# Kernel optimization log

Hardware: AMD Instinct MI355X
Metric: run time of the kernel (lower is better)

The kernel has to match this reference:

```python
import jax, jax.numpy as jnp
import numpy as np

AX = (-2, -1)
LAMBDA = 0.05
ITERS = 6

# torch fft_2d_img  = fftshift(ifft2(ifftshift(x)))  (used in the FORWARD model)
# torch ifft_2d_img = ifftshift(fft2(fftshift(x)))   (used in the ADJOINT model)

def _fwd_xform(x):
    return jnp.fft.fftshift(jnp.fft.ifft2(jnp.fft.ifftshift(x, axes=AX), axes=AX, norm='ortho'), axes=AX)

def _adj_xform(x):
    return jnp.fft.ifftshift(jnp.fft.fft2(jnp.fft.fftshift(x, axes=AX), axes=AX, norm='ortho'), axes=AX)

def _forward_model(img, S, mask):
    # img [b,t,h,w] -> masked multicoil k-space [b,t,c,h,w]
    return mask * _fwd_xform(S * img[:, :, None])

def _adjoint_model(k, S):
    # k [b,t,c,h,w] -> coil-combined image [b,t,h,w]
    return jnp.sum(jnp.conj(S) * _adj_xform(k), axis=2)

def _system_matrix_R(p, S, L, mask):
    # p [b,sv,h,w]; L [b,t,sv]
    expanded = jnp.einsum('bts,bshw->bthw', L, p)
    combined = _adjoint_model(_forward_model(expanded, S, mask), S)
    out = jnp.einsum('bts,bthw->bshw', jnp.conj(L), combined)
    return out + LAMBDA * p

def _cg_solve(b_vec, S, L, mask):
    z0 = jnp.zeros_like(b_vec)
    rs0 = jnp.vdot(b_vec, b_vec)

    def step(carry, _):
        z, r, p, rs_old, done = carry
        Ap = _system_matrix_R(p, S, L, mask)
        alpha = rs_old / (jnp.vdot(p, Ap) + 1e-20)
        z_n = z + alpha * p
        r_n = r - alpha * Ap
        rs_new = jnp.vdot(r_n, r_n)
        p_n = r_n + (rs_new / (rs_old + 1e-20)) * p
        # replicate torch early-break: freeze state once residual is tiny
        z_o = jnp.where(done, z, z_n)
        r_o = jnp.where(done, r, r_n)
        p_o = jnp.where(done, p, p_n)
        rs_o = jnp.where(done, rs_old, rs_new)
        done_n = done | (jnp.abs(rs_o) < 1e-10)
        return (z_o, r_o, p_o, rs_o, done_n), None

    carry0 = (z0, b_vec, b_vec, rs0, jnp.array(False))
    (z, _, _, _, _), _ = jax.lax.scan(step, carry0, None, length=ITERS)
    return z

def setup_inputs() -> dict:
    key = jax.random.key(0)
    ks = jax.random.split(key, 9)
    b, t, c, h, w, sv = 2, 12, 10, 256, 256, 3
    f32 = jnp.float32
    inp = {
        'k_real': jax.random.normal(ks[0], (b, t, c, h, w), f32),
        'k_imag': jax.random.normal(ks[1], (b, t, c, h, w), f32),
        'mo_real': jax.random.normal(ks[2], (b, sv, h, w), f32),
        'mo_imag': jax.random.normal(ks[3], (b, sv, h, w), f32),
        's_real': jax.random.normal(ks[4], (b, 1, c, h, w), f32),
        's_imag': jax.random.normal(ks[5], (b, 1, c, h, w), f32),
        'tb_real': jax.random.normal(ks[6], (b, t, sv), f32),
        'tb_imag': jax.random.normal(ks[7], (b, t, sv), f32),
        'mask': (jax.random.uniform(ks[8], (b, t, 1, h, w)) < 0.35).astype(f32),
    }
    return inp

def reference(k_real, k_imag, mo_real, mo_imag, s_real, s_imag, tb_real, tb_imag, mask):
    Y = k_real + 1j * k_imag          # [b,t,c,h,w]
    MO = mo_real + 1j * mo_imag       # [b,sv,h,w]
    S = s_real + 1j * s_imag          # [b,1,c,h,w]
    L = tb_real + 1j * tb_imag        # [b,t,sv]
    # b = L^H A^H Y + lambda * model_output
    b_vec = jnp.einsum('bts,bthw->bshw', jnp.conj(L), _adjoint_model(Y, S)) + LAMBDA * MO
    z = _cg_solve(b_vec, S, L, mask)  # [b,sv,h,w] complex
    return jnp.stack([z.real, z.imag], axis=-1)  # [b,sv,h,w,2] float32
```

## Files before the change

kernel.cpp:

```cpp
#include <hip/hip_runtime.h>
#include <math.h>

#define HW 65536
#define LAM 0.05f

struct Scal {
  double pap_re, pap_im, rs_acc, rs_old;
  int done, cnt;
};

__device__ __forceinline__ float2 cadd(float2 a, float2 b){ return make_float2(a.x+b.x, a.y+b.y); }
__device__ __forceinline__ float2 csub(float2 a, float2 b){ return make_float2(a.x-b.x, a.y-b.y); }
__device__ __forceinline__ float2 cmul(float2 a, float2 b){
  return make_float2(a.x*b.x - a.y*b.y, a.x*b.y + a.y*b.x);
}
__device__ __forceinline__ float2 cmulj(float2 a, float2 b){
  return make_float2(a.x*b.x + a.y*b.y, a.x*b.y - a.y*b.x);
}
__device__ __forceinline__ int swz(int p){ return p ^ (p>>4); }

__device__ __forceinline__ void wave_lds_sync(){
  __builtin_amdgcn_wave_barrier();
  __asm__ __volatile__("s_waitcnt lgkmcnt(0)" ::: "memory");
  __builtin_amdgcn_wave_barrier();
}

template<int S>
__device__ __forceinline__ void bfly4(float2 x0, float2 x1, float2 x2, float2 x3,
                                      float2& y0, float2& y1, float2& y2, float2& y3){
  float2 a  = cadd(x0,x2), bm = csub(x0,x2);
  float2 c  = cadd(x1,x3), d  = csub(x1,x3);
  float2 jd = make_float2(-(float)S*d.y, (float)S*d.x);
  y0 = cadd(a,c); y2 = csub(a,c); y1 = cadd(bm,jd); y3 = csub(bm,jd);
}

template<int S>
__device__ __forceinline__ void dft16(float2* a){
  const float s_ = (float)S;
  const float2 W1 = make_float2( 0.92387953251f,  s_*0.38268343236f);
  const float2 W2 = make_float2( 0.70710678119f,  s_*0.70710678119f);
  const float2 W3 = make_float2( 0.38268343236f,  s_*0.92387953251f);
  const float2 W4_ = make_float2(0.f,              s_*1.f);
  const float2 W6 = make_float2(-0.70710678119f,  s_*0.70710678119f);
  const float2 W9 = make_float2(-0.92387953251f, -s_*0.38268343236f);
  float2 t[16];
#pragma unroll
  for (int n0=0;n0<4;n0++){
    float2 y0,y1,y2,y3;
    bfly4<S>(a[n0], a[n0+4], a[n0+8], a[n0+12], y0,y1,y2,y3);
    if (n0==1){ y1=cmul(y1,W1); y2=cmul(y2,W2); y3=cmul(y3,W3); }
    if (n0==2){ y1=cmul(y1,W2); y2=cmul(y2,W4_); y3=cmul(y3,W6); }
    if (n0==3){ y1=cmul(y1,W3); y2=cmul(y2,W6); y3=cmul(y3,W9); }
    t[n0*4+0]=y0; t[n0*4+1]=y1; t[n0*4+2]=y2; t[n0*4+3]=y3;
  }
#pragma unroll
  for (int k1=0;k1<4;k1++){
    float2 y0,y1,y2,y3;
    bfly4<S>(t[0*4+k1], t[1*4+k1], t[2*4+k1], t[3*4+k1], y0,y1,y2,y3);
    a[k1+0]=y0; a[k1+4]=y1; a[k1+8]=y2; a[k1+12]=y3;
  }
}

template<int S>
__device__ void fft256_r16(float2* buf, int l){
  float2 a[16];
#pragma unroll
  for (int j=0;j<16;j++) a[j] = buf[swz(l + 16*j)];
  dft16<S>(a);
  float ang = (float)S * 6.2831853071795865f * (float)l * (1.f/256.f);
  float sn, cs; __sincosf(ang, &sn, &cs);
  float2 wstep = make_float2(cs, sn);
  float2 w = wstep;
#pragma unroll
  for (int k=1;k<16;k++){ a[k] = cmul(a[k], w); w = cmul(w, wstep); }
#pragma unroll
  for (int k=0;k<16;k++) buf[swz(16*k + l)] = a[k];
  wave_lds_sync();
#pragma unroll
  for (int j=0;j<16;j++) a[j] = buf[swz(16*l + j)];
  dft16<S>(a);
  wave_lds_sync();
#pragma unroll
  for (int k=0;k<16;k++) buf[swz(l + 16*k)] = a[k];
  wave_lds_sync();
}

__global__ __launch_bounds__(256) void k_w(const float* __restrict__ mask,
                                           const float* __restrict__ tbr,
                                           const float* __restrict__ tbi,
                                           float2* __restrict__ Wb,
                                           Scal* sc){
  if (blockIdx.x==0 && blockIdx.y==0 && threadIdx.x==0){
    sc->pap_re=0.0; sc->pap_im=0.0; sc->rs_acc=0.0; sc->rs_old=0.0;
    sc->done=0; sc->cnt=0;
  }
  __shared__ float2 wt[9][16][17];
  int tid = threadIdx.x;
  int bx = blockIdx.x;
  int b  = blockIdx.y;
  int u0 = (bx>>4)<<4, v0 = (bx&15)<<4;
  int u_l = tid>>4, v_l = tid&15;
  int pix = (u0+u_l)*256 + (v0+v_l);
  float d0=0,d1=0,d2=0, o01r=0,o01i=0, o02r=0,o02i=0, o12r=0,o12i=0;
#pragma unroll
  for (int t=0;t<12;t++){
    float m = mask[(size_t)(b*12+t)*HW + pix];
    int lb = (b*12+t)*3;
    float l0r = tbr[lb+0], l0i = tbi[lb+0];
    float l1r = tbr[lb+1], l1i = tbi[lb+1];
    float l2r = tbr[lb+2], l2i = tbi[lb+2];
    d0 += m*(l0r*l0r + l0i*l0i);
    d1 += m*(l1r*l1r + l1i*l1i);
    d2 += m*(l2r*l2r + l2i*l2i);
    o01r += m*(l0r*l1r + l0i*l1i); o01i += m*(l0r*l1i - l0i*l1r);
    o02r += m*(l0r*l2r + l0i*l2i); o02i += m*(l0r*l2i - l0i*l2r);
    o12r += m*(l1r*l2r + l1i*l2i); o12i += m*(l1r*l2i - l1i*l2r);
  }
  const float s = 1.0f/65536.0f;
  wt[0][u_l][v_l] = make_float2(d0*s, 0.f);
  wt[1][u_l][v_l] = make_float2(o01r*s,  o01i*s);
  wt[2][u_l][v_l] = make_float2(o02r*s,  o02i*s);
  wt[3][u_l][v_l] = make_float2(o01r*s, -o01i*s);
  wt[4][u_l][v_l] = make_float2(d1*s, 0.f);
  wt[5][u_l][v_l] = make_float2(o12r*s,  o12i*s);
  wt[6][u_l][v_l] = make_float2(o02r*s, -o02i*s);
  wt[7][u_l][v_l] = make_float2(o12r*s, -o12i*s);
  wt[8][u_l][v_l] = make_float2(d2*s, 0.f);
  __syncthreads();
  int u_l2 = tid&15, v_l2 = tid>>4;
#pragma unroll
  for (int k=0;k<9;k++){
    Wb[ ((size_t)(b*9+k)*256 + (v0+v_l2))*256 + (u0+u_l2) ] = wt[k][u_l2][v_l2];
  }
}

__global__ __launch_bounds__(512) void k_yrow(const float* __restrict__ kr,
                                              const float* __restrict__ ki,
                                              const float* __restrict__ tbr,
                                              const float* __restrict__ tbi,
                                              float2* __restrict__ bufA){
  __shared__ float2 lb[30*257];
  int tid = threadIdx.x;
  int wv = tid>>6, lane = tid&63, g = lane>>4, l = lane&15;
  int px = tid & 255, half = tid >> 8;
  int r = blockIdx.x, b = blockIdx.y;
  float sg = (((r ^ px) & 1) ? -1.f : 1.f) * (1.f/256.f);
  int sk = swz(px);
#pragma unroll
  for (int cc=0; cc<5; cc++){
    int c = half*5 + cc;
    float a0r=0,a0i=0,a1r=0,a1i=0,a2r=0,a2i=0;
#pragma unroll
    for (int t=0;t<12;t++){
      size_t off = ((size_t)((b*12+t)*10+c))*HW + (size_t)r*256 + px;
      float yr = kr[off], yi = ki[off];
      int lbi = (b*12+t)*3;
      float l0r = tbr[lbi+0], l0i = tbi[lbi+0];
      float l1r = tbr[lbi+1], l1i = tbi[lbi+1];
      float l2r = tbr[lbi+2], l2i = tbi[lbi+2];
      a0r += l0r*yr + l0i*yi;  a0i += l0r*yi - l0i*yr;
      a1r += l1r*yr + l1i*yi;  a1i += l1r*yi - l1i*yr;
      a2r += l2r*yr + l2i*yi;  a2i += l2r*yi - l2i*yr;
    }
    lb[(c*3+0)*257 + sk] = make_float2(a0r*sg, a0i*sg);
    lb[(c*3+1)*257 + sk] = make_float2(a1r*sg, a1i*sg);
    lb[(c*3+2)*257 + sk] = make_float2(a2r*sg, a2i*sg);
  }
  __syncthreads();
  int tau = 4*wv + g;
  if (tau < 30){
    float2* lw = &lb[tau*257];
    fft256_r16<-1>(lw, l);
    float2* dst = bufA + (size_t)(b*30+tau)*HW + (size_t)r*256;
#pragma unroll
    for (int j=0;j<8;j++){
      int e = 2*(16*j + l);
      float2 e0 = lw[swz(e)], e1 = lw[swz(e+1)];
      *(float4*)(dst + e) = make_float4(e0.x,e0.y,e1.x,e1.y);
    }
  }
}

template<int MODE>
__global__ __launch_bounds__(384) void k_colpass(float2* __restrict__ bufA,
                                                 const float2* __restrict__ Wb){
  __shared__ float2 lb[24*257];
  int tid = threadIdx.x;
  int wv = tid>>6, lane = tid&63, g = lane>>4, l = lane&15;
  int j0 = blockIdx.x*8;
  int c = blockIdx.y, b = blockIdx.z;
#pragma unroll
  for (int it=0; it<8; it++){
    int idx = it*384 + tid;
    int s = idx>>10, rem = idx&1023, u = rem>>2, cp = rem&3;
    const float2* src = bufA + (size_t)(b*30 + c*3 + s)*HW;
    float4 v = *(const float4*)(src + u*256 + j0 + 2*cp);
    lb[(s*8+2*cp  )*257 + swz(u)] = make_float2(v.x, v.y);
    lb[(s*8+2*cp+1)*257 + swz(u)] = make_float2(v.z, v.w);
  }
  __syncthreads();
  int tau = 4*wv + g;
  if (MODE==0){
    fft256_r16<-1>(&lb[tau*257], l);
  } else {
    fft256_r16<1>(&lb[tau*257], l);
    __syncthreads();
    const float2* Wp = Wb + (size_t)b*9*HW;
    for (int idx=tid; idx<2048; idx+=384){
      int u = idx&255, col = idx>>8;
      int su = swz(u);
      int v = j0 + col;
      float2 x0 = lb[(0*8+col)*257 + su];
      float2 x1 = lb[(1*8+col)*257 + su];
      float2 x2 = lb[(2*8+col)*257 + su];
      size_t wb = (size_t)v*256 + u;
      float2 y0 = cmul(Wp[(size_t)0*HW + wb], x0);
      y0 = cadd(y0, cmul(Wp[(size_t)1*HW + wb], x1));
      y0 = cadd(y0, cmul(Wp[(size_t)2*HW + wb], x2));
      float2 y1 = cmul(Wp[(size_t)3*HW + wb], x0);
      y1 = cadd(y1, cmul(Wp[(size_t)4*HW + wb], x1));
      y1 = cadd(y1, cmul(Wp[(size_t)5*HW + wb], x2));
      float2 y2 = cmul(Wp[(size_t)6*HW + wb], x0);
      y2 = cadd(y2, cmul(Wp[(size_t)7*HW + wb], x1));
      y2 = cadd(y2, cmul(Wp[(size_t)8*HW + wb], x2));
      lb[(0*8+col)*257 + su] = y0;
      lb[(1*8+col)*257 + su] = y1;
      lb[(2*8+col)*257 + su] = y2;
    }
    __syncthreads();
    fft256_r16<-1>(&lb[tau*257], l);
  }
  __syncthreads();
#pragma unroll
  for (int it=0; it<8; it++){
    int idx = it*384 + tid;
    int s = idx>>10, rem = idx&1023, u = rem>>2, cp = rem&3;
    float2* dst = bufA + (size_t)(b*30 + c*3 + s)*HW;
    float2 e0 = lb[(s*8+2*cp  )*257 + swz(u)];
    float2 e1 = lb[(s*8+2*cp+1)*257 + swz(u)];
    *(float4*)(dst + u*256 + j0 + 2*cp) = make_float4(e0.x, e0.y, e1.x, e1.y);
  }
}

__global__ __launch_bounds__(256) void k_combine(const float2* __restrict__ bufA,
                                                 const float* __restrict__ sr_,
                                                 const float* __restrict__ si_,
                                                 const float* __restrict__ mor,
                                                 const float* __restrict__ moi,
                                                 float2* __restrict__ bvec,
                                                 Scal* sc){
  __shared__ double sd[4];
  int tid = threadIdx.x;
  int i = blockIdx.x*256 + tid;
  int pix = i & (HW-1);
  int bs = i >> 16;
  int b = bs/3, s = bs - 3*b;
  float2 acc = make_float2(0.f, 0.f);
#pragma unroll
  for (int c=0;c<10;c++){
    float2 F  = bufA[(size_t)(b*30 + c*3 + s)*HW + pix];
    size_t so = (size_t)(b*10+c)*HW + pix;
    float2 sv = make_float2(sr_[so], si_[so]);
    acc = cadd(acc, cmulj(sv, F));
  }
  float sgl = (((pix>>8)^pix)&1 ? -1.f : 1.f) * LAM;
  acc.x += sgl*mor[i]; acc.y += sgl*moi[i];
  bvec[i] = acc;
  double dre = (double)acc.x*acc.x + (double)acc.y*acc.y;
  for (int off=32; off>0; off>>=1) dre += __shfl_down(dre, off, 64);
  if ((tid&63)==0) sd[tid>>6] = dre;
  __syncthreads();
  if (tid==0) atomicAdd(&sc->rs_acc, sd[0]+sd[1]+sd[2]+sd[3]);
}

__global__ __launch_bounds__(512) void k_spfft(float2* __restrict__ p,
                                               const float2* __restrict__ rvec,
                                               const float* __restrict__ sr_,
                                               const float* __restrict__ si_,
                                               float2* __restrict__ bufA,
                                               Scal* sc, int first){
  __shared__ float2 lb[30*257];
  int tid = threadIdx.x;
  int wv = tid>>6, lane = tid&63, g = lane>>4, l = lane&15;
  int r = blockIdx.x, b = blockIdx.y;
  if (tid < 256){
    int px = tid, sk = swz(px);
    int done = sc->done;
    float beta = first ? 0.f : (float)(sc->rs_acc / (sc->rs_old + 1e-20));
    float2 pv[3];
#pragma unroll
    for (int s=0;s<3;s++){
      size_t oi = (size_t)(b*3+s)*HW + (size_t)r*256 + px;
      if (!first && !done){
        float2 po = p[oi], rv = rvec[oi];
        float2 pn = make_float2(rv.x + beta*po.x, rv.y + beta*po.y);
        p[oi] = pn; pv[s] = pn;
      } else {
        pv[s] = p[oi];
      }
    }
#pragma unroll
    for (int c=0;c<10;c++){
      size_t so = (size_t)(b*10+c)*HW + (size_t)r*256 + px;
      float2 sv = make_float2(sr_[so], si_[so]);
      lb[(c*3+0)*257 + sk] = cmul(sv, pv[0]);
      lb[(c*3+1)*257 + sk] = cmul(sv, pv[1]);
      lb[(c*3+2)*257 + sk] = cmul(sv, pv[2]);
    }
  }
  __syncthreads();
  int tau = 4*wv + g;
  if (tau < 30){
    float2* lw = &lb[tau*257];
    fft256_r16<1>(lw, l);
    float2* dst = bufA + (size_t)(b*30+tau)*HW + (size_t)r*256;
#pragma unroll
    for (int j=0;j<8;j++){
      int e = 2*(16*j + l);
      float2 e0 = lw[swz(e)], e1 = lw[swz(e+1)];
      *(float4*)(dst + e) = make_float4(e0.x,e0.y,e1.x,e1.y);
    }
  }
  if (tid==0){
    int total = (int)(gridDim.x*gridDim.y);
    int prev = atomicAdd(&sc->cnt, 1);
    if (prev == total-1){
      sc->cnt = 0;
      if (!first && !sc->done){
        sc->rs_old = sc->rs_acc;
        if (fabs(sc->rs_old) < 1e-10) sc->done = 1;
      }
      sc->pap_re = 0.0; sc->pap_im = 0.0; sc->rs_acc = 0.0;
    }
  }
}

__global__ __launch_bounds__(512) void k_rowcomb(const float2* __restrict__ bufA,
                                                 const float* __restrict__ sr_,
                                                 const float* __restrict__ si_,
                                                 const float2* __restrict__ pvec,
                                                 float2* __restrict__ Ap,
                                                 Scal* sc){
  __shared__ float2 lb[30*257];
  __shared__ double sd[8], sd2[8];
  int tid = threadIdx.x;
  int wv = tid>>6, lane = tid&63, g = lane>>4, l = lane&15;
  int r = blockIdx.x, b = blockIdx.y;
  int tau = 4*wv + g;
  if (tau < 30){
    const float2* src = bufA + (size_t)(b*30+tau)*HW + (size_t)r*256;
    float2* lw = &lb[tau*257];
#pragma unroll
    for (int j=0;j<8;j++){
      int e = 2*(16*j + l);
      float4 v = *(const float4*)(src + e);
      lw[swz(e)]   = make_float2(v.x, v.y);
      lw[swz(e+1)] = make_float2(v.z, v.w);
    }
    wave_lds_sync();
    fft256_r16<-1>(lw, l);
  }
  __syncthreads();
  double dre = 0.0, dim = 0.0;
  if (tid < 256){
    int px = tid, sk = swz(px);
    float2 a0={0,0}, a1={0,0}, a2={0,0};
#pragma unroll
    for (int c=0;c<10;c++){
      size_t so = (size_t)(b*10+c)*HW + (size_t)r*256 + px;
      float2 sv = make_float2(sr_[so], si_[so]);
      a0 = cadd(a0, cmulj(sv, lb[(c*3+0)*257 + sk]));
      a1 = cadd(a1, cmulj(sv, lb[(c*3+1)*257 + sk]));
      a2 = cadd(a2, cmulj(sv, lb[(c*3+2)*257 + sk]));
    }
    float2 accs[3] = {a0,a1,a2};
#pragma unroll
    for (int s=0;s<3;s++){
      size_t oi = (size_t)(b*3+s)*HW + (size_t)r*256 + px;
      float2 acc = accs[s];
      float2 av = pvec[oi];
      acc.x += LAM*av.x; acc.y += LAM*av.y;
      Ap[oi] = acc;
      dre += (double)av.x*acc.x + (double)av.y*acc.y;
      dim += (double)av.x*acc.y - (double)av.y*acc.x;
    }
  }
  for (int off=32; off>0; off>>=1){
    dre += __shfl_down(dre, off, 64);
    dim += __shfl_down(dim, off, 64);
  }
  if (lane==0){ sd[wv]=dre; sd2[wv]=dim; }
  __syncthreads();
  if (tid==0){
    double tre=0.0, tim=0.0;
#pragma unroll
    for (int q=0;q<8;q++){ tre+=sd[q]; tim+=sd2[q]; }
    atomicAdd(&sc->pap_re, tre);
    atomicAdd(&sc->pap_im, tim);
  }
}

__global__ __launch_bounds__(256) void k_cginit(const float2* __restrict__ bvec,
                                                float2* __restrict__ z,
                                                float2* __restrict__ r,
                                                float2* __restrict__ p,
                                                Scal* sc){
  int i = blockIdx.x*256 + threadIdx.x;
  float2 bv = bvec[i];
  z[i] = make_float2(0.f,0.f);
  r[i] = bv; p[i] = bv;
  if (i==0){ sc->rs_old = sc->rs_acc; sc->pap_re=0.0; sc->pap_im=0.0; }
}

__global__ __launch_bounds__(256) void k_upzr(float2* __restrict__ z,
                                              float2* __restrict__ r,
                                              const float2* __restrict__ p,
                                              const float2* __restrict__ Ap,
                                              Scal* sc){
  __shared__ double sd[4];
  int tid = threadIdx.x;
  int i = blockIdx.x*256 + tid;
  int done = sc->done;
  double local = 0.0;
  if (!done){
    double dre = sc->pap_re + 1e-20, dim = sc->pap_im;
    double den = dre*dre + dim*dim;
    double rs = sc->rs_old;
    float2 alpha = make_float2((float)( rs*dre/den), (float)(-rs*dim/den));
    float2 pv = p[i], apv = Ap[i];
    float2 zv = cadd(z[i], cmul(alpha, pv));
    float2 rv = csub(r[i], cmul(alpha, apv));
    z[i] = zv; r[i] = rv;
    local = (double)rv.x*rv.x + (double)rv.y*rv.y;
  }
  for (int off=32; off>0; off>>=1) local += __shfl_down(local, off, 64);
  if ((tid&63)==0) sd[tid>>6] = local;
  __syncthreads();
  if (tid==0 && !done){
    atomicAdd(&sc->rs_acc, sd[0]+sd[1]+sd[2]+sd[3]);
  }
}

__global__ __launch_bounds__(256) void k_out(const float2* __restrict__ z,
                                             float* __restrict__ out){
  int i = blockIdx.x*256 + threadIdx.x;
  int pix = i & (HW-1);
  float sgn = (((pix>>8)^pix)&1) ? -1.f : 1.f;
  float2 zv = z[i];
  out[2*i]   = sgn*zv.x;
  out[2*i+1] = sgn*zv.y;
}

extern "C" void kernel_launch(void* const* d_in, const int* in_sizes, int n_in,
                              void* d_out, int out_size, void* d_ws, size_t ws_size,
                              hipStream_t stream){
  const float* kr   = (const float*)d_in[0];
  const float* ki   = (const float*)d_in[1];
  const float* mor  = (const float*)d_in[2];
  const float* moi  = (const float*)d_in[3];
  const float* sr   = (const float*)d_in[4];
  const float* si   = (const float*)d_in[5];
  const float* tbr  = (const float*)d_in[6];
  const float* tbi  = (const float*)d_in[7];
  const float* mask = (const float*)d_in[8];
  float* out = (float*)d_out;

  float2* ws   = (float2*)d_ws;
  float2* bufA = ws;
  float2* Wb   = ws + 3932160;
  float2* bvec = ws + 5111808;
  float2* z    = ws + 5505024;
  float2* r    = ws + 5898240;
  float2* p    = ws + 6291456;
  float2* Ap   = ws + 6684672;
  Scal*   sc   = (Scal*)(ws + 7077888);

  k_w<<<dim3(256,2),dim3(256),0,stream>>>(mask, tbr, tbi, Wb, sc);
  k_yrow<<<dim3(256,2),dim3(512),0,stream>>>(kr, ki, tbr, tbi, bufA);
  k_colpass<0><<<dim3(32,10,2),dim3(384),0,stream>>>(bufA, Wb);
  k_combine<<<dim3(1536),dim3(256),0,stream>>>(bufA, sr, si, mor, moi, bvec, sc);
  k_cginit<<<dim3(1536),dim3(256),0,stream>>>(bvec, z, r, p, sc);
  for (int it=0; it<6; ++it){
    k_spfft<<<dim3(256,2),dim3(512),0,stream>>>(p, r, sr, si, bufA, sc, it==0 ? 1 : 0);
    k_colpass<1><<<dim3(32,10,2),dim3(384),0,stream>>>(bufA, Wb);
    k_rowcomb<<<dim3(256,2),dim3(512),0,stream>>>(bufA, sr, si, p, Ap, sc);
    k_upzr<<<dim3(1536),dim3(256),0,stream>>>(z, r, p, Ap, sc);
  }
  k_out<<<dim3(1536),dim3(256),0,stream>>>(z, out);
}
```

Before: 750.3 us.

## Fuse CG vector updates into spfft, compute rs_new algebraically, store Hermitian weights compactly

Removes the separate z/r update kernel and the cginit kernel. The alpha, beta and rs_new scalars are now computed in the last block of k_rowcomb from the extra dot products r·Ap and Ap·Ap, using the expansion |r-αAp|². The z/r/p updates are deferred into the next k_spfft and into k_out. The 3x3 weight matrix is stored as 9 real floats that exploit its Hermitian symmetry, instead of 9 complex values, which halves the weight reads in colpass. The algebraic rs_new can lose precision through cancellation compared with the directly computed norm.

```diff
diff --git a/kernel.cpp b/kernel.cpp
--- a/kernel.cpp
+++ b/kernel.cpp
@@ -5,8 +5,9 @@
 #define LAM 0.05f
 
 struct Scal {
-  double pap_re, pap_im, rs_acc, rs_old;
-  int done, cnt;
+  double pap_re, pap_im, rq_re, rq_im, qq;
+  double rs_old, al_re, al_im, beta;
+  int done, apply, cnt, pad;
 };
 
 __device__ __forceinline__ float2 cadd(float2 a, float2 b){ return make_float2(a.x+b.x, a.y+b.y); }
@@ -88,13 +89,14 @@
 __global__ __launch_bounds__(256) void k_w(const float* __restrict__ mask,
                                            const float* __restrict__ tbr,
                                            const float* __restrict__ tbi,
-                                           float2* __restrict__ Wb,
+                                           float* __restrict__ Wf,
                                            Scal* sc){
   if (blockIdx.x==0 && blockIdx.y==0 && threadIdx.x==0){
-    sc->pap_re=0.0; sc->pap_im=0.0; sc->rs_acc=0.0; sc->rs_old=0.0;
-    sc->done=0; sc->cnt=0;
-  }
-  __shared__ float2 wt[9][16][17];
+    sc->pap_re=0.0; sc->pap_im=0.0; sc->rq_re=0.0; sc->rq_im=0.0; sc->qq=0.0;
+    sc->rs_old=0.0; sc->al_re=0.0; sc->al_im=0.0; sc->beta=0.0;
+    sc->done=0; sc->apply=0; sc->cnt=0;
+  }
+  __shared__ float wtf[9][16][17];
   int tid = threadIdx.x;
   int bx = blockIdx.x;
   int b  = blockIdx.y;
@@ -117,20 +119,15 @@
     o12r += m*(l1r*l2r + l1i*l2i); o12i += m*(l1r*l2i - l1i*l2r);
   }
   const float s = 1.0f/65536.0f;
-  wt[0][u_l][v_l] = make_float2(d0*s, 0.f);
-  wt[1][u_l][v_l] = make_float2(o01r*s,  o01i*s);
-  wt[2][u_l][v_l] = make_float2(o02r*s,  o02i*s);
-  wt[3][u_l][v_l] = make_float2(o01r*s, -o01i*s);
-  wt[4][u_l][v_l] = make_float2(d1*s, 0.f);
-  wt[5][u_l][v_l] = make_float2(o12r*s,  o12i*s);
-  wt[6][u_l][v_l] = make_float2(o02r*s, -o02i*s);
-  wt[7][u_l][v_l] = make_float2(o12r*s, -o12i*s);
-  wt[8][u_l][v_l] = make_float2(d2*s, 0.f);
+  wtf[0][u_l][v_l] = d0*s;   wtf[1][u_l][v_l] = d1*s;   wtf[2][u_l][v_l] = d2*s;
+  wtf[3][u_l][v_l] = o01r*s; wtf[4][u_l][v_l] = o01i*s;
+  wtf[5][u_l][v_l] = o02r*s; wtf[6][u_l][v_l] = o02i*s;
+  wtf[7][u_l][v_l] = o12r*s; wtf[8][u_l][v_l] = o12i*s;
   __syncthreads();
   int u_l2 = tid&15, v_l2 = tid>>4;
 #pragma unroll
-  for (int k=0;k<9;k++){
-    Wb[ ((size_t)(b*9+k)*256 + (v0+v_l2))*256 + (u0+u_l2) ] = wt[k][u_l2][v_l2];
+  for (int f=0;f<9;f++){
+    Wf[ ((size_t)(b*9+f)*256 + (v0+v_l2))*256 + (u0+u_l2) ] = wtf[f][u_l2][v_l2];
   }
 }
 
@@ -183,7 +180,7 @@
 
 template<int MODE>
 __global__ __launch_bounds__(384) void k_colpass(float2* __restrict__ bufA,
-                                                 const float2* __restrict__ Wb){
+                                                 const float* __restrict__ Wf){
   __shared__ float2 lb[24*257];
   int tid = threadIdx.x;
   int wv = tid>>6, lane = tid&63, g = lane>>4, l = lane&15;
@@ -205,7 +202,7 @@
   } else {
     fft256_r16<1>(&lb[tau*257], l);
     __syncthreads();
-    const float2* Wp = Wb + (size_t)b*9*HW;
+    const float* W0 = Wf + (size_t)b*9*HW;
     for (int idx=tid; idx<2048; idx+=384){
       int u = idx&255, col = idx>>8;
       int su = swz(u);
@@ -214,15 +211,19 @@
       float2 x1 = lb[(1*8+col)*257 + su];
       float2 x2 = lb[(2*8+col)*257 + su];
       size_t wb = (size_t)v*256 + u;
-      float2 y0 = cmul(Wp[(size_t)0*HW + wb], x0);
-      y0 = cadd(y0, cmul(Wp[(size_t)1*HW + wb], x1));
-      y0 = cadd(y0, cmul(Wp[(size_t)2*HW + wb], x2));
-      float2 y1 = cmul(Wp[(size_t)3*HW + wb], x0);
-      y1 = cadd(y1, cmul(Wp[(size_t)4*HW + wb], x1));
-      y1 = cadd(y1, cmul(Wp[(size_t)5*HW + wb], x2));
-      float2 y2 = cmul(Wp[(size_t)6*HW + wb], x0);
-      y2 = cadd(y2, cmul(Wp[(size_t)7*HW + wb], x1));
-      y2 = cadd(y2, cmul(Wp[(size_t)8*HW + wb], x2));
+      float d0  = W0[(size_t)0*HW + wb];
+      float d1  = W0[(size_t)1*HW + wb];
+      float d2  = W0[(size_t)2*HW + wb];
+      float o01r= W0[(size_t)3*HW + wb], o01i = W0[(size_t)4*HW + wb];
+      float o02r= W0[(size_t)5*HW + wb], o02i = W0[(size_t)6*HW + wb];
+      float o12r= W0[(size_t)7*HW + wb], o12i = W0[(size_t)8*HW + wb];
+      float2 y0, y1, y2;
+      y0.x = d0*x0.x + o01r*x1.x - o01i*x1.y + o02r*x2.x - o02i*x2.y;
+      y0.y = d0*x0.y + o01r*x1.y + o01i*x1.x + o02r*x2.y + o02i*x2.x;
+      y1.x = o01r*x0.x + o01i*x0.y + d1*x1.x + o12r*x2.x - o12i*x2.y;
+      y1.y = o01r*x0.y - o01i*x0.x + d1*x1.y + o12r*x2.y + o12i*x2.x;
+      y2.x = o02r*x0.x + o02i*x0.y + o12r*x1.x + o12i*x1.y + d2*x2.x;
+      y2.y = o02r*x0.y - o02i*x0.x + o12r*x1.y - o12i*x1.x + d2*x2.y;
       lb[(0*8+col)*257 + su] = y0;
       lb[(1*8+col)*257 + su] = y1;
       lb[(2*8+col)*257 + su] = y2;
@@ -247,7 +248,9 @@
                                                  const float* __restrict__ si_,
                                                  const float* __restrict__ mor,
                                                  const float* __restrict__ moi,
-                                                 float2* __restrict__ bvec,
+                                                 float2* __restrict__ z,
+                                                 float2* __restrict__ r,
+                                                 float2* __restrict__ p,
                                                  Scal* sc){
   __shared__ double sd[4];
   int tid = threadIdx.x;
@@ -265,39 +268,46 @@
   }
   float sgl = (((pix>>8)^pix)&1 ? -1.f : 1.f) * LAM;
   acc.x += sgl*mor[i]; acc.y += sgl*moi[i];
-  bvec[i] = acc;
+  z[i] = make_float2(0.f,0.f);
+  r[i] = acc; p[i] = acc;
   double dre = (double)acc.x*acc.x + (double)acc.y*acc.y;
   for (int off=32; off>0; off>>=1) dre += __shfl_down(dre, off, 64);
   if ((tid&63)==0) sd[tid>>6] = dre;
   __syncthreads();
-  if (tid==0) atomicAdd(&sc->rs_acc, sd[0]+sd[1]+sd[2]+sd[3]);
+  if (tid==0) atomicAdd(&sc->rs_old, sd[0]+sd[1]+sd[2]+sd[3]);
 }
 
 __global__ __launch_bounds__(512) void k_spfft(float2* __restrict__ p,
-                                               const float2* __restrict__ rvec,
+                                               float2* __restrict__ rvec,
+                                               float2* __restrict__ z,
+                                               const float2* __restrict__ Ap,
                                                const float* __restrict__ sr_,
                                                const float* __restrict__ si_,
                                                float2* __restrict__ bufA,
-                                               Scal* sc, int first){
+                                               Scal* sc){
   __shared__ float2 lb[30*257];
   int tid = threadIdx.x;
   int wv = tid>>6, lane = tid&63, g = lane>>4, l = lane&15;
   int r = blockIdx.x, b = blockIdx.y;
   if (tid < 256){
     int px = tid, sk = swz(px);
-    int done = sc->done;
-    float beta = first ? 0.f : (float)(sc->rs_acc / (sc->rs_old + 1e-20));
+    int ap = sc->apply;
+    float2 alpha = make_float2((float)sc->al_re, (float)sc->al_im);
+    float beta = (float)sc->beta;
     float2 pv[3];
 #pragma unroll
     for (int s=0;s<3;s++){
       size_t oi = (size_t)(b*3+s)*HW + (size_t)r*256 + px;
-      if (!first && !done){
-        float2 po = p[oi], rv = rvec[oi];
-        float2 pn = make_float2(rv.x + beta*po.x, rv.y + beta*po.y);
-        p[oi] = pn; pv[s] = pn;
-      } else {
-        pv[s] = p[oi];
+      float2 pvv = p[oi];
+      if (ap){
+        float2 zv = z[oi], rv = rvec[oi], apv = Ap[oi];
+        zv = cadd(zv, cmul(alpha, pvv));
+        rv = csub(rv, cmul(alpha, apv));
+        float2 pn = make_float2(rv.x + beta*pvv.x, rv.y + beta*pvv.y);
+        z[oi] = zv; rvec[oi] = rv; p[oi] = pn;
+        pvv = pn;
       }
+      pv[s] = pvv;
     }
 #pragma unroll
     for (int c=0;c<10;c++){
@@ -321,28 +331,17 @@
       *(float4*)(dst + e) = make_float4(e0.x,e0.y,e1.x,e1.y);
     }
   }
-  if (tid==0){
-    int total = (int)(gridDim.x*gridDim.y);
-    int prev = atomicAdd(&sc->cnt, 1);
-    if (prev == total-1){
-      sc->cnt = 0;
-      if (!first && !sc->done){
-        sc->rs_old = sc->rs_acc;
-        if (fabs(sc->rs_old) < 1e-10) sc->done = 1;
-      }
-      sc->pap_re = 0.0; sc->pap_im = 0.0; sc->rs_acc = 0.0;
-    }
-  }
 }
 
 __global__ __launch_bounds__(512) void k_rowcomb(const float2* __restrict__ bufA,
                                                  const float* __restrict__ sr_,
                                                  const float* __restrict__ si_,
                                                  const float2* __restrict__ pvec,
+                                                 const float2* __restrict__ rvec,
                                                  float2* __restrict__ Ap,
                                                  Scal* sc){
   __shared__ float2 lb[30*257];
-  __shared__ double sd[8], sd2[8];
+  __shared__ double sd[5][8];
   int tid = threadIdx.x;
   int wv = tid>>6, lane = tid&63, g = lane>>4, l = lane&15;
   int r = blockIdx.x, b = blockIdx.y;
@@ -361,7 +360,7 @@
     fft256_r16<-1>(lw, l);
   }
   __syncthreads();
-  double dre = 0.0, dim = 0.0;
+  double d0=0.0, d1=0.0, d2=0.0, d3=0.0, d4=0.0;
   if (tid < 256){
     int px = tid, sk = swz(px);
     float2 a0={0,0}, a1={0,0}, a2={0,0};
@@ -379,74 +378,68 @@
       size_t oi = (size_t)(b*3+s)*HW + (size_t)r*256 + px;
       float2 acc = accs[s];
       float2 av = pvec[oi];
+      float2 rv = rvec[oi];
       acc.x += LAM*av.x; acc.y += LAM*av.y;
       Ap[oi] = acc;
-      dre += (double)av.x*acc.x + (double)av.y*acc.y;
-      dim += (double)av.x*acc.y - (double)av.y*acc.x;
+      d0 += (double)av.x*acc.x + (double)av.y*acc.y;
+      d1 += (double)av.x*acc.y - (double)av.y*acc.x;
+      d2 += (double)rv.x*acc.x + (double)rv.y*acc.y;
+      d3 += (double)rv.x*acc.y - (double)rv.y*acc.x;
+      d4 += (double)acc.x*acc.x + (double)acc.y*acc.y;
     }
   }
   for (int off=32; off>0; off>>=1){
-    dre += __shfl_down(dre, off, 64);
-    dim += __shfl_down(dim, off, 64);
-  }
-  if (lane==0){ sd[wv]=dre; sd2[wv]=dim; }
+    d0 += __shfl_down(d0, off, 64);
+    d1 += __shfl_down(d1, off, 64);
+    d2 += __shfl_down(d2, off, 64);
+    d3 += __shfl_down(d3, off, 64);
+    d4 += __shfl_down(d4, off, 64);
+  }
+  if (lane==0){ sd[0][wv]=d0; sd[1][wv]=d1; sd[2][wv]=d2; sd[3][wv]=d3; sd[4][wv]=d4; }
   __syncthreads();
   if (tid==0){
-    double tre=0.0, tim=0.0;
-#pragma unroll
-    for (int q=0;q<8;q++){ tre+=sd[q]; tim+=sd2[q]; }
-    atomicAdd(&sc->pap_re, tre);
-    atomicAdd(&sc->pap_im, tim);
-  }
-}
-
-__global__ __launch_bounds__(256) void k_cginit(const float2* __restrict__ bvec,
-                                                float2* __restrict__ z,
-                                                float2* __restrict__ r,
-                                                float2* __restrict__ p,
-                                                Scal* sc){
-  int i = blockIdx.x*256 + threadIdx.x;
-  float2 bv = bvec[i];
-  z[i] = make_float2(0.f,0.f);
-  r[i] = bv; p[i] = bv;
-  if (i==0){ sc->rs_old = sc->rs_acc; sc->pap_re=0.0; sc->pap_im=0.0; }
-}
-
-__global__ __launch_bounds__(256) void k_upzr(float2* __restrict__ z,
-                                              float2* __restrict__ r,
-                                              const float2* __restrict__ p,
-                                              const float2* __restrict__ Ap,
-                                              Scal* sc){
-  __shared__ double sd[4];
-  int tid = threadIdx.x;
-  int i = blockIdx.x*256 + tid;
-  int done = sc->done;
-  double local = 0.0;
-  if (!done){
-    double dre = sc->pap_re + 1e-20, dim = sc->pap_im;
-    double den = dre*dre + dim*dim;
-    double rs = sc->rs_old;
-    float2 alpha = make_float2((float)( rs*dre/den), (float)(-rs*dim/den));
-    float2 pv = p[i], apv = Ap[i];
-    float2 zv = cadd(z[i], cmul(alpha, pv));
-    float2 rv = csub(r[i], cmul(alpha, apv));
-    z[i] = zv; r[i] = rv;
-    local = (double)rv.x*rv.x + (double)rv.y*rv.y;
-  }
-  for (int off=32; off>0; off>>=1) local += __shfl_down(local, off, 64);
-  if ((tid&63)==0) sd[tid>>6] = local;
-  __syncthreads();
-  if (tid==0 && !done){
-    atomicAdd(&sc->rs_acc, sd[0]+sd[1]+sd[2]+sd[3]);
+    double t0=0,t1=0,t2=0,t3=0,t4=0;
+#pragma unroll
+    for (int q=0;q<8;q++){ t0+=sd[0][q]; t1+=sd[1][q]; t2+=sd[2][q]; t3+=sd[3][q]; t4+=sd[4][q]; }
+    atomicAdd(&sc->pap_re, t0); atomicAdd(&sc->pap_im, t1);
+    atomicAdd(&sc->rq_re,  t2); atomicAdd(&sc->rq_im,  t3);
+    atomicAdd(&sc->qq,     t4);
+    int total = (int)(gridDim.x*gridDim.y);
+    int prev = atomicAdd(&sc->cnt, 1);
+    if (prev == total-1){
+      sc->cnt = 0;
+      if (!sc->done){
+        double pr = sc->pap_re + 1e-20, pi = sc->pap_im;
+        double den = pr*pr + pi*pi;
+        double rs = sc->rs_old;
+        double alr =  rs*pr/den, ali = -rs*pi/den;
+        double rs_new = rs - 2.0*(alr*sc->rq_re - ali*sc->rq_im)
+                           + (alr*alr + ali*ali)*sc->qq;
+        sc->al_re = alr; sc->al_im = ali;
+        sc->beta = rs_new/(rs + 1e-20);
+        sc->rs_old = rs_new;
+        sc->apply = 1;
+        if (fabs(rs_new) < 1e-10) sc->done = 1;
+      } else {
+        sc->apply = 0;
+      }
+      sc->pap_re=0.0; sc->pap_im=0.0; sc->rq_re=0.0; sc->rq_im=0.0; sc->qq=0.0;
+    }
   }
 }
 
 __global__ __launch_bounds__(256) void k_out(const float2* __restrict__ z,
+                                             const float2* __restrict__ p,
+                                             const Scal* sc,
                                              float* __restrict__ out){
   int i = blockIdx.x*256 + threadIdx.x;
   int pix = i & (HW-1);
   float sgn = (((pix>>8)^pix)&1) ? -1.f : 1.f;
   float2 zv = z[i];
+  if (sc->apply){
+    float2 alpha = make_float2((float)sc->al_re, (float)sc->al_im);
+    zv = cadd(zv, cmul(alpha, p[i]));
+  }
   out[2*i]   = sgn*zv.x;
   out[2*i+1] = sgn*zv.y;
 }
@@ -467,24 +460,22 @@
 
   float2* ws   = (float2*)d_ws;
   float2* bufA = ws;
-  float2* Wb   = ws + 3932160;
-  float2* bvec = ws + 5111808;
-  float2* z    = ws + 5505024;
-  float2* r    = ws + 5898240;
-  float2* p    = ws + 6291456;
-  float2* Ap   = ws + 6684672;
-  Scal*   sc   = (Scal*)(ws + 7077888);
-
-  k_w<<<dim3(256,2),dim3(256),0,stream>>>(mask, tbr, tbi, Wb, sc);
+  float*  Wf   = (float*)(ws + 3932160);
+  float2* z    = ws + 4521984;
+  float2* r    = ws + 4915200;
+  float2* p    = ws + 5308416;
+  float2* Ap   = ws + 5701632;
+  Scal*   sc   = (Scal*)(ws + 6094848);
+
+  k_w<<<dim3(256,2),dim3(256),0,stream>>>(mask, tbr, tbi, Wf, sc);
   k_yrow<<<dim3(256,2),dim3(512),0,stream>>>(kr, ki, tbr, tbi, bufA);
-  k_colpass<0><<<dim3(32,10,2),dim3(384),0,stream>>>(bufA, Wb);
-  k_combine<<<dim3(1536),dim3(256),0,stream>>>(bufA, sr, si, mor, moi, bvec, sc);
-  k_cginit<<<dim3(1536),dim3(256),0,stream>>>(bvec, z, r, p, sc);
+  k_colpass<0><<<dim3(32,10,2),dim3(384),0,stream>>>(bufA, Wf);
+  k_combine<<<dim3(1536),dim3(256),0,stream>>>(bufA, sr, si, mor, moi,
+                                               z, r, p, sc);
   for (int it=0; it<6; ++it){
-    k_spfft<<<dim3(256,2),dim3(512),0,stream>>>(p, r, sr, si, bufA, sc, it==0 ? 1 : 0);
-    k_colpass<1><<<dim3(32,10,2),dim3(384),0,stream>>>(bufA, Wb);
-    k_rowcomb<<<dim3(256,2),dim3(512),0,stream>>>(bufA, sr, si, p, Ap, sc);
-    k_upzr<<<dim3(1536),dim3(256),0,stream>>>(z, r, p, Ap, sc);
-  }
-  k_out<<<dim3(1536),dim3(256),0,stream>>>(z, out);
-}
+    k_spfft<<<dim3(256,2),dim3(512),0,stream>>>(p, r, z, Ap, sr, si, bufA, sc);
+    k_colpass<1><<<dim3(32,10,2),dim3(384),0,stream>>>(bufA, Wf);
+    k_rowcomb<<<dim3(256,2),dim3(512),0,stream>>>(bufA, sr, si, p, r, Ap, sc);
+  }
+  k_out<<<dim3(1536),dim3(256),0,stream>>>(z, p, sc, out);
+}
```

Measured after the change: 726.6 us. -3.2%, faster.
